# Kernel tuning notes

Measured on AMD Instinct MI355X. Metric: run time of the kernel, lower is better.

## Reference

```python
import jax, jax.numpy as jnp
import numpy as np

BN_EPS = 1e-5
ATT_EPS = 1e-6


def _conv(x, w, groups=1):
    # x: [B,C,H,W], w: [O, C//groups, k, k], stride 1, SAME padding for odd k
    k = w.shape[-1]
    p = (k - 1) // 2
    return jax.lax.conv_general_dilated(
        x, w, window_strides=(1, 1), padding=[(p, p), (p, p)],
        dimension_numbers=('NCHW', 'OIHW', 'NCHW'), feature_group_count=groups)


def _bn(x, bnp):
    # bnp: [4, C] stacked (scale, bias, running_mean, running_var); eval-mode BN
    s, b, m, v = bnp[0], bnp[1], bnp[2], bnp[3]
    inv = s / jnp.sqrt(v + BN_EPS)
    return x * inv[None, :, None, None] + (b - m * inv)[None, :, None, None]


def _relu6(x):
    return jnp.clip(x, 0.0, 6.0)


def _ffn(x, fc1_w, fc1_bn, conv1_w, conv1_bn, conv2_w, conv2_bn, fc2_w, fc2_bn):
    # E_FFN: 1x1 ConvBNReLU6 -> dw5x5 ConvBNReLU6 & dw3x3 ConvBNReLU6 -> sum -> 1x1 ConvBN -> ReLU6
    C = x.shape[1]
    h = _relu6(_bn(_conv(x, fc1_w), fc1_bn))
    x1 = _relu6(_bn(_conv(h, conv1_w, groups=C), conv1_bn))
    x2 = _relu6(_bn(_conv(h, conv2_w, groups=C), conv2_bn))
    return _relu6(_bn(_conv(x1 + x2, fc2_w), fc2_bn))


def _bias(y, b):
    return y + b[None, :, None, None]


def setup_inputs() -> dict:
    key = jax.random.key(0)
    ks = jax.random.split(key, 16)
    C, M = 64, 8  # in_places, in_places // scale
    B, H, W = 4, 224, 224

    def w(k, shape, s=0.05):
        return (jax.random.normal(k, shape, dtype=jnp.float32) * s)

    def bn_params(k, c):
        k1, k2, k3, k4 = jax.random.split(k, 4)
        scale = 1.0 + 0.1 * jax.random.normal(k1, (c,), dtype=jnp.float32)
        bias = 0.1 * jax.random.normal(k2, (c,), dtype=jnp.float32)
        mean = 0.1 * jax.random.normal(k3, (c,), dtype=jnp.float32)
        var = 1.0 + 0.1 * jax.random.uniform(k4, (c,), dtype=jnp.float32)
        return jnp.stack([scale, bias, mean, var])  # [4, c]

    return {
        'x': jax.random.normal(ks[0], (B, C, H, W), dtype=jnp.float32),
        'gamma': jnp.full((1,), 0.5, dtype=jnp.float32),  # nonzero so attention branch matters
        'q_w': w(ks[1], (M, C, 1, 1)), 'q_b': w(ks[2], (M,)),
        'k_w': w(ks[3], (M, C, 1, 1)), 'k_b': w(ks[4], (M,)),
        'v_w': w(ks[5], (C, C, 1, 1)), 'v_b': w(ks[6], (C,)),
        'fc1_w': w(ks[7], (C, C, 1, 1)), 'fc1_bn': bn_params(ks[8], C),
        'conv1_w': w(ks[9], (C, 1, 5, 5)), 'conv1_bn': bn_params(ks[10], C),
        'conv2_w': w(ks[11], (C, 1, 3, 3)), 'conv2_bn': bn_params(ks[12], C),
        'fc2_w': w(ks[13], (C, C, 1, 1)), 'fc2_bn': bn_params(ks[14], C),
    }


def reference(x, gamma, q_w, q_b, k_w, k_b, v_w, v_b,
              fc1_w, fc1_bn, conv1_w, conv1_bn, conv2_w, conv2_bn, fc2_w, fc2_bn):
    B, C, H, W = x.shape
    N = H * W
    x_channel = _ffn(x, fc1_w, fc1_bn, conv1_w, conv1_bn, conv2_w, conv2_bn, fc2_w, fc2_bn)
    # softplus feature maps; Q,K: [B, m, N]
    Q = jax.nn.softplus(_bias(_conv(x, q_w), q_b).reshape(B, -1, N))
    K = jax.nn.softplus(_bias(_conv(x, k_w), k_b).reshape(B, -1, N))
    V = (_bias(_conv(x, v_w), v_b) + x_channel).reshape(B, C, N)
    Qt = jnp.swapaxes(Q, 1, 2)                              # [B, N, m]
    KV = jnp.einsum('bmn,bcn->bmc', K, V)                   # [B, m, C]
    norm = 1.0 / jnp.einsum('bnm,bm->bn', Qt, K.sum(-1) + ATT_EPS)  # [B, N]
    wv = jnp.einsum('bnm,bmc,bn->bcn', Qt, KV, norm).reshape(B, C, H, W)
    return x + gamma * wv
```

## Files before the change

kernel.cpp:

```cpp
#include <hip/hip_runtime.h>
#include <math.h>

#define B_ 4
#define C_ 64
#define M_ 8
#define H_ 224
#define W_ 224
#define N_ (H_*W_)
#define CN_ (C_*N_)
#define MN_ (M_*N_)
#define BCN_ (B_*CN_)
#define BMN_ (B_*MN_)

__device__ __forceinline__ float relu6f(float v){ return fminf(fmaxf(v,0.0f),6.0f); }
__device__ __forceinline__ float softplusf(float v){
  return v > 0.0f ? v + log1pf(expf(-v)) : log1pf(expf(v));
}

__global__ __launch_bounds__(256) void k_fc1k(const float* __restrict__ x,
                                              const float* __restrict__ w,
                                              const float* __restrict__ bn,
                                              const float* __restrict__ kw,
                                              const float* __restrict__ kb,
                                              float* __restrict__ h,
                                              float* __restrict__ Kq)
{
  __shared__ float wt[64*64];
  __shared__ float kt[64*8];
  const int tid = threadIdx.x;
  for (int idx = tid; idx < 4096; idx += 256) {
    const int c = idx >> 6, o = idx & 63;
    wt[idx] = w[o*64 + c];
  }
  for (int idx = tid; idx < 512; idx += 256) {
    const int c = idx >> 3, m = idx & 7;
    kt[idx] = kw[m*64 + c];
  }
  __syncthreads();

  const int lane = tid & 63, wave = tid >> 6;
  const int b  = blockIdx.x / 196;
  const int pg = blockIdx.x % 196;
  const int pix = pg*256 + 4*lane;
  const float* xb = x + (size_t)b*CN_ + pix;
  const int ob = wave*16;

  float4 acc[16];
  float4 ak0 = {0,0,0,0}, ak1 = {0,0,0,0};
  #pragma unroll
  for (int i = 0; i < 16; ++i) acc[i] = make_float4(0.f,0.f,0.f,0.f);

  #pragma unroll 2
  for (int c = 0; c < 64; ++c) {
    const float4 xv = *(const float4*)(xb + (size_t)c*N_);
    const float* wc = &wt[c*64 + ob];
    const float2 k2 = *(const float2*)&kt[c*8 + wave*2];
    #pragma unroll
    for (int o = 0; o < 16; ++o) {
      const float wv = wc[o];
      acc[o].x = fmaf(wv, xv.x, acc[o].x);
      acc[o].y = fmaf(wv, xv.y, acc[o].y);
      acc[o].z = fmaf(wv, xv.z, acc[o].z);
      acc[o].w = fmaf(wv, xv.w, acc[o].w);
    }
    ak0.x = fmaf(k2.x, xv.x, ak0.x); ak0.y = fmaf(k2.x, xv.y, ak0.y);
    ak0.z = fmaf(k2.x, xv.z, ak0.z); ak0.w = fmaf(k2.x, xv.w, ak0.w);
    ak1.x = fmaf(k2.y, xv.x, ak1.x); ak1.y = fmaf(k2.y, xv.y, ak1.y);
    ak1.z = fmaf(k2.y, xv.z, ak1.z); ak1.w = fmaf(k2.y, xv.w, ak1.w);
  }

  float* hb = h + (size_t)b*CN_ + pix;
  #pragma unroll
  for (int o = 0; o < 16; ++o) {
    const int oc = ob + o;
    const float inv  = bn[oc] / sqrtf(bn[192+oc] + 1e-5f);
    const float beta = bn[64+oc] - bn[128+oc]*inv;
    float4 o4;
    o4.x = relu6f(fmaf(acc[o].x, inv, beta));
    o4.y = relu6f(fmaf(acc[o].y, inv, beta));
    o4.z = relu6f(fmaf(acc[o].z, inv, beta));
    o4.w = relu6f(fmaf(acc[o].w, inv, beta));
    *(float4*)(hb + (size_t)oc*N_) = o4;
  }
  const int m0 = wave*2;
  const float kb0 = kb[m0], kb1 = kb[m0+1];
  float* Kb = Kq + (size_t)b*MN_ + pix;
  float4 q0, q1;
  q0.x = softplusf(ak0.x+kb0); q0.y = softplusf(ak0.y+kb0);
  q0.z = softplusf(ak0.z+kb0); q0.w = softplusf(ak0.w+kb0);
  q1.x = softplusf(ak1.x+kb1); q1.y = softplusf(ak1.y+kb1);
  q1.z = softplusf(ak1.z+kb1); q1.w = softplusf(ak1.w+kb1);
  *(float4*)(Kb + (size_t)m0*N_)     = q0;
  *(float4*)(Kb + (size_t)(m0+1)*N_) = q1;
}

__global__ __launch_bounds__(256) void k_dw(const float* __restrict__ h,
                                            const float* __restrict__ w5,
                                            const float* __restrict__ w3,
                                            const float* __restrict__ bn1,
                                            const float* __restrict__ bn2,
                                            float* __restrict__ s)
{
  __shared__ float tile[36*37];
  const int tid = threadIdx.x;
  const int blk = blockIdx.x;
  const int t   = blk % 49;
  const int bc  = blk / 49;
  const int c   = bc & 63;
  const int tx0 = (t % 7) * 32;
  const int ty0 = (t / 7) * 32;
  const float* hb = h + (size_t)bc * N_;

  for (int idx = tid; idx < 1296; idx += 256) {
    const int ly = idx / 36, lx = idx - ly*36;
    const int gy = ty0 + ly - 2, gx = tx0 + lx - 2;
    float v = 0.0f;
    if (gy >= 0 && gy < H_ && gx >= 0 && gx < W_) v = hb[gy*W_ + gx];
    tile[ly*37 + lx] = v;
  }
  __syncthreads();

  float w5r[25], w3r[9];
  #pragma unroll
  for (int i = 0; i < 25; ++i) w5r[i] = w5[c*25 + i];
  #pragma unroll
  for (int i = 0; i < 9; ++i)  w3r[i] = w3[c*9 + i];
  const float inv1 = bn1[c] / sqrtf(bn1[192+c] + 1e-5f);
  const float bet1 = bn1[64+c] - bn1[128+c]*inv1;
  const float inv2 = bn2[c] / sqrtf(bn2[192+c] + 1e-5f);
  const float bet2 = bn2[64+c] - bn2[128+c]*inv2;

  const int ty  = tid >> 3;
  const int tx4 = (tid & 7) << 2;
  float a5[4] = {0,0,0,0}, a3[4] = {0,0,0,0};
  #pragma unroll
  for (int dy = 0; dy < 5; ++dy) {
    float r[8];
    #pragma unroll
    for (int i = 0; i < 8; ++i) r[i] = tile[(ty+dy)*37 + tx4 + i];
    #pragma unroll
    for (int dx = 0; dx < 5; ++dx) {
      const float wv = w5r[dy*5+dx];
      #pragma unroll
      for (int p = 0; p < 4; ++p) a5[p] = fmaf(wv, r[p+dx], a5[p]);
    }
    if (dy >= 1 && dy <= 3) {
      #pragma unroll
      for (int dx = 1; dx <= 3; ++dx) {
        const float wv = w3r[(dy-1)*3+(dx-1)];
        #pragma unroll
        for (int p = 0; p < 4; ++p) a3[p] = fmaf(wv, r[p+dx], a3[p]);
      }
    }
  }
  float* sb = s + (size_t)bc * N_ + (ty0+ty)*W_ + tx0 + tx4;
  float4 o4;
  o4.x = relu6f(fmaf(a5[0],inv1,bet1)) + relu6f(fmaf(a3[0],inv2,bet2));
  o4.y = relu6f(fmaf(a5[1],inv1,bet1)) + relu6f(fmaf(a3[1],inv2,bet2));
  o4.z = relu6f(fmaf(a5[2],inv1,bet1)) + relu6f(fmaf(a3[2],inv2,bet2));
  o4.w = relu6f(fmaf(a5[3],inv1,bet1)) + relu6f(fmaf(a3[3],inv2,bet2));
  *(float4*)sb = o4;
}

__global__ __launch_bounds__(256) void k_v(const float* __restrict__ x,
                                           const float* __restrict__ s,
                                           const float* __restrict__ vw,
                                           const float* __restrict__ vb,
                                           const float* __restrict__ fw,
                                           const float* __restrict__ fbn,
                                           float* __restrict__ V)
{
  __shared__ float wtv[64*64];
  __shared__ float wtf[64*64];
  const int tid = threadIdx.x;
  for (int idx = tid; idx < 4096; idx += 256) {
    const int c = idx >> 6, o = idx & 63;
    wtv[idx] = vw[o*64 + c];
    wtf[idx] = fw[o*64 + c];
  }
  __syncthreads();

  const int lane = tid & 63, wave = tid >> 6;
  const int b  = blockIdx.x / 196;
  const int pg = blockIdx.x % 196;
  const int pix = pg*256 + 4*lane;
  const float* xb = x + (size_t)b*CN_ + pix;
  const float* sb = s + (size_t)b*CN_ + pix;
  const int ob = wave*16;

  float4 av[16], af[16];
  #pragma unroll
  for (int i = 0; i < 16; ++i) { av[i] = make_float4(0,0,0,0); af[i] = make_float4(0,0,0,0); }

  #pragma unroll 2
  for (int c = 0; c < 64; ++c) {
    const float4 xv = *(const float4*)(xb + (size_t)c*N_);
    const float4 sv = *(const float4*)(sb + (size_t)c*N_);
    const float* wvc = &wtv[c*64 + ob];
    const float* wfc = &wtf[c*64 + ob];
    #pragma unroll
    for (int o = 0; o < 16; ++o) {
      const float a = wvc[o];
      const float f = wfc[o];
      av[o].x = fmaf(a, xv.x, av[o].x);
      av[o].y = fmaf(a, xv.y, av[o].y);
      av[o].z = fmaf(a, xv.z, av[o].z);
      av[o].w = fmaf(a, xv.w, av[o].w);
      af[o].x = fmaf(f, sv.x, af[o].x);
      af[o].y = fmaf(f, sv.y, af[o].y);
      af[o].z = fmaf(f, sv.z, af[o].z);
      af[o].w = fmaf(f, sv.w, af[o].w);
    }
  }

  float* Vb = V + (size_t)b*CN_ + pix;
  #pragma unroll
  for (int o = 0; o < 16; ++o) {
    const int oc = ob + o;
    const float inv  = fbn[oc] / sqrtf(fbn[192+oc] + 1e-5f);
    const float beta = fbn[64+oc] - fbn[128+oc]*inv;
    const float bias = vb[oc];
    float4 o4;
    o4.x = av[o].x + bias + relu6f(fmaf(af[o].x, inv, beta));
    o4.y = av[o].y + bias + relu6f(fmaf(af[o].y, inv, beta));
    o4.z = av[o].z + bias + relu6f(fmaf(af[o].z, inv, beta));
    o4.w = av[o].w + bias + relu6f(fmaf(af[o].w, inv, beta));
    *(float4*)(Vb + (size_t)oc*N_) = o4;
  }
}

__global__ __launch_bounds__(256) void k_kv(const float* __restrict__ V,
                                            const float* __restrict__ Kq,
                                            float* __restrict__ KV,
                                            float* __restrict__ Ksum)
{
  const int blk = blockIdx.x;
  const int b   = blk >> 7;
  const int rem = blk & 127;
  const int cg  = rem >> 4;
  const int ch  = rem & 15;
  const int tid = threadIdx.x;
  const int base = ch * 3136;
  const int end  = base + 3136;
  const float* Kb = Kq + (size_t)b*MN_;
  const float* Vb = V  + (size_t)b*CN_ + (size_t)(cg*8)*N_;

  float acc[64];
  #pragma unroll
  for (int i = 0; i < 64; ++i) acc[i] = 0.0f;
  float ks[8] = {0,0,0,0,0,0,0,0};

  for (int n = base + tid; n < end; n += 256) {
    float kv[8];
    #pragma unroll
    for (int m2 = 0; m2 < 8; ++m2) kv[m2] = Kb[m2*N_ + n];
    #pragma unroll
    for (int m2 = 0; m2 < 8; ++m2) ks[m2] += kv[m2];
    #pragma unroll
    for (int c8 = 0; c8 < 8; ++c8) {
      const float vv = Vb[c8*N_ + n];
      #pragma unroll
      for (int m2 = 0; m2 < 8; ++m2)
        acc[m2*8+c8] = fmaf(kv[m2], vv, acc[m2*8+c8]);
    }
  }
  const int lane = tid & 63;
  float mine = 0.0f;
  #pragma unroll
  for (int jj = 0; jj < 64; ++jj) {
    float v = acc[jj];
    v += __shfl_xor(v, 1);
    v += __shfl_xor(v, 2);
    v += __shfl_xor(v, 4);
    v += __shfl_xor(v, 8);
    v += __shfl_xor(v, 16);
    v += __shfl_xor(v, 32);
    if (lane == jj) mine = v;
  }
  atomicAdd(&KV[b*512 + (lane>>3)*64 + cg*8 + (lane&7)], mine);
  if (cg == 0) {
    float mk = 0.0f;
    #pragma unroll
    for (int jj = 0; jj < 8; ++jj) {
      float v = ks[jj];
      v += __shfl_xor(v, 1);
      v += __shfl_xor(v, 2);
      v += __shfl_xor(v, 4);
      v += __shfl_xor(v, 8);
      v += __shfl_xor(v, 16);
      v += __shfl_xor(v, 32);
      if (lane == jj) mk = v;
    }
    if (lane < 8) atomicAdd(&Ksum[b*8 + lane], mk);
  }
}

__global__ __launch_bounds__(256) void k_out(const float* __restrict__ x,
                                             const float* __restrict__ qw,
                                             const float* __restrict__ qb,
                                             const float* __restrict__ gamma,
                                             const float* __restrict__ KV,
                                             const float* __restrict__ Ksum,
                                             float* __restrict__ out)
{
  __shared__ float xs[64*256];
  __shared__ __align__(16) float kvt[64*8];
  __shared__ __align__(16) float wqt[64*8];
  __shared__ float ksl[8];
  const int tid = threadIdx.x;
  const int b  = blockIdx.x / 196;
  const int pg = blockIdx.x % 196;
  const int pix0 = pg*256;
  const float* xb = x + (size_t)b*CN_ + pix0;

  for (int idx = tid; idx < 512; idx += 256) {
    const int m = idx >> 6, c = idx & 63;
    kvt[c*8 + m] = KV[b*512 + idx];
    wqt[c*8 + m] = qw[idx];
  }
  if (tid < 8) ksl[tid] = Ksum[b*8 + tid] + 1e-6f;
  for (int idx = tid; idx < 4096; idx += 256) {
    const int c = idx >> 6, i = idx & 63;
    const float4 v = ((const float4*)(xb + (size_t)c*N_))[i];
    ((float4*)&xs[c*256])[i] = v;
  }
  __syncthreads();

  float q[8] = {0,0,0,0,0,0,0,0};
  #pragma unroll 8
  for (int c = 0; c < 64; ++c) {
    const float xv = xs[c*256 + tid];
    const float4 w0 = *(const float4*)&wqt[c*8];
    const float4 w1 = *(const float4*)&wqt[c*8+4];
    q[0] = fmaf(w0.x, xv, q[0]);
    q[1] = fmaf(w0.y, xv, q[1]);
    q[2] = fmaf(w0.z, xv, q[2]);
    q[3] = fmaf(w0.w, xv, q[3]);
    q[4] = fmaf(w1.x, xv, q[4]);
    q[5] = fmaf(w1.y, xv, q[5]);
    q[6] = fmaf(w1.z, xv, q[6]);
    q[7] = fmaf(w1.w, xv, q[7]);
  }
  float den = 0.0f;
  #pragma unroll
  for (int m = 0; m < 8; ++m) {
    q[m] = softplusf(q[m] + qb[m]);
    den  = fmaf(q[m], ksl[m], den);
  }
  const float sc = gamma[0] / den;

  float* ob = out + (size_t)b*CN_ + pix0 + tid;
  #pragma unroll 8
  for (int c = 0; c < 64; ++c) {
    const float xv = xs[c*256 + tid];
    const float4 k0 = *(const float4*)&kvt[c*8];
    const float4 k1 = *(const float4*)&kvt[c*8+4];
    float wv;
    wv = q[0]*k0.x;
    wv = fmaf(q[1], k0.y, wv);
    wv = fmaf(q[2], k0.z, wv);
    wv = fmaf(q[3], k0.w, wv);
    wv = fmaf(q[4], k1.x, wv);
    wv = fmaf(q[5], k1.y, wv);
    wv = fmaf(q[6], k1.z, wv);
    wv = fmaf(q[7], k1.w, wv);
    ob[(size_t)c*N_] = fmaf(sc, wv, xs[c*256 + tid]);
  }
}

extern "C" void kernel_launch(void* const* d_in, const int* in_sizes, int n_in,
                              void* d_out, int out_size, void* d_ws, size_t ws_size,
                              hipStream_t stream) {
  const float* x      = (const float*)d_in[0];
  const float* gamma  = (const float*)d_in[1];
  const float* q_w    = (const float*)d_in[2];
  const float* q_b    = (const float*)d_in[3];
  const float* k_w    = (const float*)d_in[4];
  const float* k_b    = (const float*)d_in[5];
  const float* v_w    = (const float*)d_in[6];
  const float* v_b    = (const float*)d_in[7];
  const float* fc1_w  = (const float*)d_in[8];
  const float* fc1_bn = (const float*)d_in[9];
  const float* c1_w   = (const float*)d_in[10];
  const float* c1_bn  = (const float*)d_in[11];
  const float* c2_w   = (const float*)d_in[12];
  const float* c2_bn  = (const float*)d_in[13];
  const float* fc2_w  = (const float*)d_in[14];
  const float* fc2_bn = (const float*)d_in[15];
  float* outp = (float*)d_out;

  float* ws   = (float*)d_ws;
  float* bufA = ws;
  float* bufS = ws + (size_t)BCN_;
  float* bufK = ws + (size_t)2*BCN_;
  float* kv   = ws + (size_t)2*BCN_ + BMN_;
  float* ksum = kv + 2048;

  hipMemsetAsync(kv, 0, (2048 + 32)*sizeof(float), stream);

  k_fc1k<<<dim3(B_*196), dim3(256), 0, stream>>>(x, fc1_w, fc1_bn, k_w, k_b, bufA, bufK);
  k_dw  <<<dim3(B_*C_*49), dim3(256), 0, stream>>>(bufA, c1_w, c2_w, c1_bn, c2_bn, bufS);
  k_v   <<<dim3(B_*196), dim3(256), 0, stream>>>(x, bufS, v_w, v_b, fc2_w, fc2_bn, bufA);
  k_kv  <<<dim3(512), dim3(256), 0, stream>>>(bufA, bufK, kv, ksum);
  k_out <<<dim3(B_*196), dim3(256), 0, stream>>>(x, q_w, q_b, gamma, kv, ksum, outp);
}
```

Measured before the change: 368.1 us.

## Split 1x1 conv kernels over output-channel halves and prefetch next channel input

The fc1/K and V/fc2 pointwise conv kernels now launch twice as many blocks, each computing 32 of the 64 output channels. This halves per-thread accumulators and shared weight tiles and adds a register prefetch of the next input channel, with vectorized float4 weight reads from LDS. The intent is more parallelism and occupancy on a grid that previously had only 784 blocks. The cost is that every input pixel is read twice from global memory, and the K branch only runs in half the blocks, which leaves those blocks imbalanced.

```diff
diff --git a/kernel.cpp b/kernel.cpp
--- a/kernel.cpp
+++ b/kernel.cpp
@@ -25,12 +25,17 @@
                                               float* __restrict__ h,
                                               float* __restrict__ Kq)
 {
-  __shared__ float wt[64*64];
-  __shared__ float kt[64*8];
-  const int tid = threadIdx.x;
-  for (int idx = tid; idx < 4096; idx += 256) {
-    const int c = idx >> 6, o = idx & 63;
-    wt[idx] = w[o*64 + c];
+  __shared__ __align__(16) float wt[64*32];
+  __shared__ __align__(16) float kt[64*8];
+  const int tid  = threadIdx.x;
+  const int b    = blockIdx.x / 392;
+  const int rem  = blockIdx.x % 392;
+  const int pg   = rem >> 1;
+  const int half = rem & 1;
+
+  for (int idx = tid; idx < 2048; idx += 256) {
+    const int c = idx >> 5, o = idx & 31;
+    wt[idx] = w[(half*32 + o)*64 + c];
   }
   for (int idx = tid; idx < 512; idx += 256) {
     const int c = idx >> 3, m = idx & 7;
@@ -39,39 +44,44 @@
   __syncthreads();
 
   const int lane = tid & 63, wave = tid >> 6;
-  const int b  = blockIdx.x / 196;
-  const int pg = blockIdx.x % 196;
   const int pix = pg*256 + 4*lane;
   const float* xb = x + (size_t)b*CN_ + pix;
-  const int ob = wave*16;
-
-  float4 acc[16];
+  const int obl = wave*8;
+  const int ob  = half*32 + obl;
+
+  float4 acc[8];
   float4 ak0 = {0,0,0,0}, ak1 = {0,0,0,0};
   #pragma unroll
-  for (int i = 0; i < 16; ++i) acc[i] = make_float4(0.f,0.f,0.f,0.f);
-
-  #pragma unroll 2
+  for (int i = 0; i < 8; ++i) acc[i] = make_float4(0.f,0.f,0.f,0.f);
+
+  float4 xv = *(const float4*)xb;
+  #pragma unroll 4
   for (int c = 0; c < 64; ++c) {
-    const float4 xv = *(const float4*)(xb + (size_t)c*N_);
-    const float* wc = &wt[c*64 + ob];
+    const size_t nxt = (c < 63) ? (size_t)(c+1)*N_ : (size_t)63*N_;
+    const float4 xn = *(const float4*)(xb + nxt);
+    const float4 w0 = *(const float4*)&wt[c*32 + obl];
+    const float4 w1 = *(const float4*)&wt[c*32 + obl + 4];
     const float2 k2 = *(const float2*)&kt[c*8 + wave*2];
-    #pragma unroll
-    for (int o = 0; o < 16; ++o) {
-      const float wv = wc[o];
-      acc[o].x = fmaf(wv, xv.x, acc[o].x);
-      acc[o].y = fmaf(wv, xv.y, acc[o].y);
-      acc[o].z = fmaf(wv, xv.z, acc[o].z);
-      acc[o].w = fmaf(wv, xv.w, acc[o].w);
-    }
-    ak0.x = fmaf(k2.x, xv.x, ak0.x); ak0.y = fmaf(k2.x, xv.y, ak0.y);
-    ak0.z = fmaf(k2.x, xv.z, ak0.z); ak0.w = fmaf(k2.x, xv.w, ak0.w);
-    ak1.x = fmaf(k2.y, xv.x, ak1.x); ak1.y = fmaf(k2.y, xv.y, ak1.y);
-    ak1.z = fmaf(k2.y, xv.z, ak1.z); ak1.w = fmaf(k2.y, xv.w, ak1.w);
+    const float wv[8] = {w0.x,w0.y,w0.z,w0.w,w1.x,w1.y,w1.z,w1.w};
+    #pragma unroll
+    for (int o = 0; o < 8; ++o) {
+      acc[o].x = fmaf(wv[o], xv.x, acc[o].x);
+      acc[o].y = fmaf(wv[o], xv.y, acc[o].y);
+      acc[o].z = fmaf(wv[o], xv.z, acc[o].z);
+      acc[o].w = fmaf(wv[o], xv.w, acc[o].w);
+    }
+    if (half == 0) {
+      ak0.x = fmaf(k2.x, xv.x, ak0.x); ak0.y = fmaf(k2.x, xv.y, ak0.y);
+      ak0.z = fmaf(k2.x, xv.z, ak0.z); ak0.w = fmaf(k2.x, xv.w, ak0.w);
+      ak1.x = fmaf(k2.y, xv.x, ak1.x); ak1.y = fmaf(k2.y, xv.y, ak1.y);
+      ak1.z = fmaf(k2.y, xv.z, ak1.z); ak1.w = fmaf(k2.y, xv.w, ak1.w);
+    }
+    xv = xn;
   }
 
   float* hb = h + (size_t)b*CN_ + pix;
   #pragma unroll
-  for (int o = 0; o < 16; ++o) {
+  for (int o = 0; o < 8; ++o) {
     const int oc = ob + o;
     const float inv  = bn[oc] / sqrtf(bn[192+oc] + 1e-5f);
     const float beta = bn[64+oc] - bn[128+oc]*inv;
@@ -82,16 +92,18 @@
     o4.w = relu6f(fmaf(acc[o].w, inv, beta));
     *(float4*)(hb + (size_t)oc*N_) = o4;
   }
-  const int m0 = wave*2;
-  const float kb0 = kb[m0], kb1 = kb[m0+1];
-  float* Kb = Kq + (size_t)b*MN_ + pix;
-  float4 q0, q1;
-  q0.x = softplusf(ak0.x+kb0); q0.y = softplusf(ak0.y+kb0);
-  q0.z = softplusf(ak0.z+kb0); q0.w = softplusf(ak0.w+kb0);
-  q1.x = softplusf(ak1.x+kb1); q1.y = softplusf(ak1.y+kb1);
-  q1.z = softplusf(ak1.z+kb1); q1.w = softplusf(ak1.w+kb1);
-  *(float4*)(Kb + (size_t)m0*N_)     = q0;
-  *(float4*)(Kb + (size_t)(m0+1)*N_) = q1;
+  if (half == 0) {
+    const int m0 = wave*2;
+    const float kb0 = kb[m0], kb1 = kb[m0+1];
+    float* Kb = Kq + (size_t)b*MN_ + pix;
+    float4 q0, q1;
+    q0.x = softplusf(ak0.x+kb0); q0.y = softplusf(ak0.y+kb0);
+    q0.z = softplusf(ak0.z+kb0); q0.w = softplusf(ak0.w+kb0);
+    q1.x = softplusf(ak1.x+kb1); q1.y = softplusf(ak1.y+kb1);
+    q1.z = softplusf(ak1.z+kb1); q1.w = softplusf(ak1.w+kb1);
+    *(float4*)(Kb + (size_t)m0*N_)     = q0;
+    *(float4*)(Kb + (size_t)(m0+1)*N_) = q1;
+  }
 }
 
 __global__ __launch_bounds__(256) void k_dw(const float* __restrict__ h,
@@ -170,52 +182,62 @@
                                            const float* __restrict__ fbn,
                                            float* __restrict__ V)
 {
-  __shared__ float wtv[64*64];
-  __shared__ float wtf[64*64];
-  const int tid = threadIdx.x;
-  for (int idx = tid; idx < 4096; idx += 256) {
-    const int c = idx >> 6, o = idx & 63;
-    wtv[idx] = vw[o*64 + c];
-    wtf[idx] = fw[o*64 + c];
+  __shared__ __align__(16) float wtv[64*32];
+  __shared__ __align__(16) float wtf[64*32];
+  const int tid  = threadIdx.x;
+  const int b    = blockIdx.x / 392;
+  const int rem  = blockIdx.x % 392;
+  const int pg   = rem >> 1;
+  const int half = rem & 1;
+
+  for (int idx = tid; idx < 2048; idx += 256) {
+    const int c = idx >> 5, o = idx & 31;
+    wtv[idx] = vw[(half*32 + o)*64 + c];
+    wtf[idx] = fw[(half*32 + o)*64 + c];
   }
   __syncthreads();
 
   const int lane = tid & 63, wave = tid >> 6;
-  const int b  = blockIdx.x / 196;
-  const int pg = blockIdx.x % 196;
   const int pix = pg*256 + 4*lane;
   const float* xb = x + (size_t)b*CN_ + pix;
   const float* sb = s + (size_t)b*CN_ + pix;
-  const int ob = wave*16;
-
-  float4 av[16], af[16];
-  #pragma unroll
-  for (int i = 0; i < 16; ++i) { av[i] = make_float4(0,0,0,0); af[i] = make_float4(0,0,0,0); }
-
-  #pragma unroll 2
+  const int obl = wave*8;
+  const int ob  = half*32 + obl;
+
+  float4 av[8], af[8];
+  #pragma unroll
+  for (int i = 0; i < 8; ++i) { av[i] = make_float4(0,0,0,0); af[i] = make_float4(0,0,0,0); }
+
+  float4 xv = *(const float4*)xb;
+  float4 sv = *(const float4*)sb;
+  #pragma unroll 4
   for (int c = 0; c < 64; ++c) {
-    const float4 xv = *(const float4*)(xb + (size_t)c*N_);
-    const float4 sv = *(const float4*)(sb + (size_t)c*N_);
-    const float* wvc = &wtv[c*64 + ob];
-    const float* wfc = &wtf[c*64 + ob];
-    #pragma unroll
-    for (int o = 0; o < 16; ++o) {
-      const float a = wvc[o];
-      const float f = wfc[o];
-      av[o].x = fmaf(a, xv.x, av[o].x);
-      av[o].y = fmaf(a, xv.y, av[o].y);
-      av[o].z = fmaf(a, xv.z, av[o].z);
-      av[o].w = fmaf(a, xv.w, av[o].w);
-      af[o].x = fmaf(f, sv.x, af[o].x);
-      af[o].y = fmaf(f, sv.y, af[o].y);
-      af[o].z = fmaf(f, sv.z, af[o].z);
-      af[o].w = fmaf(f, sv.w, af[o].w);
-    }
+    const size_t nxt = (c < 63) ? (size_t)(c+1)*N_ : (size_t)63*N_;
+    const float4 xn = *(const float4*)(xb + nxt);
+    const float4 sn = *(const float4*)(sb + nxt);
+    const float4 a0 = *(const float4*)&wtv[c*32 + obl];
+    const float4 a1 = *(const float4*)&wtv[c*32 + obl + 4];
+    const float4 f0 = *(const float4*)&wtf[c*32 + obl];
+    const float4 f1 = *(const float4*)&wtf[c*32 + obl + 4];
+    const float wa[8] = {a0.x,a0.y,a0.z,a0.w,a1.x,a1.y,a1.z,a1.w};
+    const float wf[8] = {f0.x,f0.y,f0.z,f0.w,f1.x,f1.y,f1.z,f1.w};
+    #pragma unroll
+    for (int o = 0; o < 8; ++o) {
+      av[o].x = fmaf(wa[o], xv.x, av[o].x);
+      av[o].y = fmaf(wa[o], xv.y, av[o].y);
+      av[o].z = fmaf(wa[o], xv.z, av[o].z);
+      av[o].w = fmaf(wa[o], xv.w, av[o].w);
+      af[o].x = fmaf(wf[o], sv.x, af[o].x);
+      af[o].y = fmaf(wf[o], sv.y, af[o].y);
+      af[o].z = fmaf(wf[o], sv.z, af[o].z);
+      af[o].w = fmaf(wf[o], sv.w, af[o].w);
+    }
+    xv = xn; sv = sn;
   }
 
   float* Vb = V + (size_t)b*CN_ + pix;
   #pragma unroll
-  for (int o = 0; o < 16; ++o) {
+  for (int o = 0; o < 8; ++o) {
     const int oc = ob + o;
     const float inv  = fbn[oc] / sqrtf(fbn[192+oc] + 1e-5f);
     const float beta = fbn[64+oc] - fbn[128+oc]*inv;
@@ -352,7 +374,6 @@
   float* ob = out + (size_t)b*CN_ + pix0 + tid;
   #pragma unroll 8
   for (int c = 0; c < 64; ++c) {
-    const float xv = xs[c*256 + tid];
     const float4 k0 = *(const float4*)&kvt[c*8];
     const float4 k1 = *(const float4*)&kvt[c*8+4];
     float wv;
@@ -398,9 +419,9 @@
 
   hipMemsetAsync(kv, 0, (2048 + 32)*sizeof(float), stream);
 
-  k_fc1k<<<dim3(B_*196), dim3(256), 0, stream>>>(x, fc1_w, fc1_bn, k_w, k_b, bufA, bufK);
+  k_fc1k<<<dim3(B_*392), dim3(256), 0, stream>>>(x, fc1_w, fc1_bn, k_w, k_b, bufA, bufK);
   k_dw  <<<dim3(B_*C_*49), dim3(256), 0, stream>>>(bufA, c1_w, c2_w, c1_bn, c2_bn, bufS);
-  k_v   <<<dim3(B_*196), dim3(256), 0, stream>>>(x, bufS, v_w, v_b, fc2_w, fc2_bn, bufA);
+  k_v   <<<dim3(B_*392), dim3(256), 0, stream>>>(x, bufS, v_w, v_b, fc2_w, fc2_bn, bufA);
   k_kv  <<<dim3(512), dim3(256), 0, stream>>>(bufA, bufK, kv, ksum);
   k_out <<<dim3(B_*196), dim3(256), 0, stream>>>(x, q_w, q_b, gamma, kv, ksum, outp);
 }
```

Result: no change. 365.6 us (-0.7%).
